# Kernel tuning notes

Hardware: AMD Instinct MI355X
Metric: run time of the kernel (lower is better)

The kernel has to match this reference:

```python
import jax, jax.numpy as jnp
import numpy as np

EMB = 128
N_RBF = 16
N_EDGES = 1_000_000
N_ATOMS = 50_000


def setup_inputs() -> dict:
    key = jax.random.key(0)
    ks = jax.random.split(key, 16)
    inp = {
        "x": jax.random.normal(ks[0], (N_EDGES, EMB), dtype=jnp.float32),
        "rbf": jax.random.normal(ks[1], (N_EDGES, N_RBF), dtype=jnp.float32),
        "idnb_i": jax.random.randint(ks[2], (N_EDGES,), 0, N_ATOMS, dtype=jnp.int32),
        "n_atoms": N_ATOMS,
        # learned params
        "W_x": jax.random.normal(ks[3], (EMB, EMB), dtype=jnp.float32) * 0.05,
        "b_x": jnp.zeros((EMB,), dtype=jnp.float32),
        "W_rbf": jax.random.normal(ks[4], (N_RBF, EMB), dtype=jnp.float32) * 0.2,
        "b_rbf": jnp.zeros((EMB,), dtype=jnp.float32),
        "W1": jax.random.normal(ks[5], (EMB, EMB), dtype=jnp.float32) * 0.05,
        "b1": jnp.zeros((EMB,), dtype=jnp.float32),
        "W2": jax.random.normal(ks[6], (EMB, EMB), dtype=jnp.float32) * 0.05,
        "b2": jnp.zeros((EMB,), dtype=jnp.float32),
        "W3": jax.random.normal(ks[7], (EMB, EMB), dtype=jnp.float32) * 0.05,
        "b3": jnp.zeros((EMB,), dtype=jnp.float32),
        "W_final": jax.random.normal(ks[8], (EMB, 1), dtype=jnp.float32) * 0.05,
        # scale coefficients (shape [1] as in the keras layer)
        "coef_rbf_a": jnp.exp(jax.random.normal(ks[9], (1,)) * 0.01),
        "coef_rbf_b": jnp.exp(jax.random.normal(ks[10], (1,)) * 0.01),
        "coef_x": jnp.exp(jax.random.normal(ks[11], (1,)) * 0.01),
        "coef_final": jnp.exp(jax.random.normal(ks[12], (1,)) * 0.01),
    }
    return inp


def reference(x, rbf, idnb_i, n_atoms, W_x, b_x, W_rbf, b_rbf, W1, b1, W2, b2,
              W3, b3, W_final, coef_rbf_a, coef_rbf_b, coef_x, coef_final):
    act = jax.nn.silu  # keras 'swish'
    rbf = coef_rbf_a * rbf
    h = act(x @ W_x + b_x)                      # [E, emb]
    g = act(rbf @ W_rbf + b_rbf)                # [E, emb]
    conv_x = (coef_rbf_b * g) * (coef_x * h)    # fused elementwise gate
    a = jax.ops.segment_sum(conv_x, idnb_i, num_segments=n_atoms)  # [n_atoms, emb]
    a = act(a @ W1 + b1)
    a = act(a @ W2 + b2)
    a = act(a @ W3 + b3)
    out = (a @ W_final) * coef_final            # [n_atoms, 1]
    return out
```

## Files before the change

### kernel.cpp

```cpp
#include <hip/hip_runtime.h>

#define E_TOTAL 1000000
#define EMB     128
#define NRBF    16
#define NATOMS  50000
#define APB     16
#define NBLK    ((NATOMS + 255) / 256)

typedef _Float16 f16x8 __attribute__((ext_vector_type(8)));
typedef _Float16 f16x4 __attribute__((ext_vector_type(4)));
typedef float    f32x4 __attribute__((ext_vector_type(4)));

__device__ __forceinline__ float silu_f(float v) {
    return v * (1.0f / (1.0f + __expf(-v)));
}

__device__ __forceinline__ int sigma64(int e) {
    return (((e & 15) >> 2) << 4) + ((e >> 4) << 2) + (e & 3);
}

__global__ __launch_bounds__(256)
void hist_kernel(const int* __restrict__ idnb, int* __restrict__ counts) {
    const int e = blockIdx.x * 256 + threadIdx.x;
    if (e < E_TOTAL) atomicAdd(&counts[idnb[e]], 1);
}

__global__ __launch_bounds__(256)
void scan1_kernel(const int* __restrict__ counts, int* __restrict__ row_ptr,
                  int* __restrict__ bsums) {
    __shared__ int sd[256];
    const int tid = threadIdx.x;
    const int idx = blockIdx.x * 256 + tid;
    const int v = (idx < NATOMS) ? counts[idx] : 0;
    sd[tid] = v;
    __syncthreads();
#pragma unroll
    for (int off = 1; off < 256; off <<= 1) {
        const int t = (tid >= off) ? sd[tid - off] : 0;
        __syncthreads();
        sd[tid] += t;
        __syncthreads();
    }
    if (idx < NATOMS) row_ptr[idx] = sd[tid] - v;
    if (tid == 255) bsums[blockIdx.x] = sd[255];
}

__global__ __launch_bounds__(256)
void scan2_kernel(int* __restrict__ bsums) {
    __shared__ int sd[256];
    const int tid = threadIdx.x;
    const int v = (tid < NBLK) ? bsums[tid] : 0;
    sd[tid] = v;
    __syncthreads();
#pragma unroll
    for (int off = 1; off < 256; off <<= 1) {
        const int t = (tid >= off) ? sd[tid - off] : 0;
        __syncthreads();
        sd[tid] += t;
        __syncthreads();
    }
    if (tid < NBLK) bsums[tid] = sd[tid] - v;
}

__global__ __launch_bounds__(256)
void scan3_kernel(const int* __restrict__ bsums, int* __restrict__ row_ptr,
                  int* __restrict__ cursor) {
    const int idx = blockIdx.x * 256 + threadIdx.x;
    if (idx < NATOMS) {
        const int r = row_ptr[idx] + bsums[blockIdx.x];
        row_ptr[idx] = r;
        cursor[idx]  = r;
    }
    if (idx == 0) row_ptr[NATOMS] = E_TOTAL;
}

__global__ __launch_bounds__(256)
void scatter_kernel(const int* __restrict__ idnb, int* __restrict__ cursor,
                    int* __restrict__ eidx) {
    const int e = blockIdx.x * 256 + threadIdx.x;
    if (e < E_TOTAL) {
        const int a = idnb[e];
        const int p = atomicAdd(&cursor[a], 1);
        eidx[p] = e;
    }
}

__global__ __launch_bounds__(256, 2)
void edge_kernel(const float* __restrict__ x,
                 const float* __restrict__ rbf,
                 const int*   __restrict__ eidx,
                 const int*   __restrict__ row_ptr,
                 const float* __restrict__ Wx,
                 const float* __restrict__ bx,
                 const float* __restrict__ Wr,
                 const float* __restrict__ br,
                 const float* __restrict__ c_a,
                 const float* __restrict__ c_b,
                 const float* __restrict__ c_x,
                 float* __restrict__ acc)
{
    __shared__ _Float16 sX[64 * 128];
    __shared__ _Float16 sR[64 * 40];
    __shared__ float    sAcc[APB][132];
    __shared__ int      sAid[64];

    const int tid  = threadIdx.x;
    const int w    = tid >> 6;
    const int lane = tid & 63;
    const int lq   = lane >> 4;
    const int lm   = lane & 15;

    const int aBase = blockIdx.x * APB;

    int rp[APB];
#pragma unroll
    for (int a = 0; a < APB; ++a) rp[a] = row_ptr[aBase + a];
    const int eBeg = rp[0];
    const int eEnd = row_ptr[aBase + APB];
    const int nEdge = eEnd - eBeg;
    const int ntile = (nEdge + 63) >> 6;

    const float ca = c_a[0];
    const float sc = c_b[0] * c_x[0];
    const int col0 = w * 32 + lm;
    const int col1 = col0 + 16;
    const float bx0 = bx[col0], bx1 = bx[col1];
    const float br0 = br[col0], br1 = br[col1];

    f16x8 wxh[4][2], wxl[4][2], wrh[2], wrl[2];
#pragma unroll
    for (int ks = 0; ks < 4; ++ks)
#pragma unroll
        for (int nt = 0; nt < 2; ++nt) {
            const int n = w * 32 + nt * 16 + lm;
            f16x8 h8, l8;
#pragma unroll
            for (int j = 0; j < 8; ++j) {
                const int k = ks * 32 + lq * 8 + j;
                const float v = Wx[k * EMB + n];
                const _Float16 hv = (_Float16)v;
                h8[j] = hv;
                l8[j] = (_Float16)(v - (float)hv);
            }
            wxh[ks][nt] = h8;
            wxl[ks][nt] = l8;
        }
#pragma unroll
    for (int nt = 0; nt < 2; ++nt) {
        const int n = w * 32 + nt * 16 + lm;
        f16x8 h8, l8;
#pragma unroll
        for (int j = 0; j < 8; ++j) {
            const int k = lq * 8 + j;
            const float v = (k < NRBF) ? Wr[k * EMB + n] : 0.f;
            const _Float16 hv = (_Float16)v;
            h8[j] = hv;
            l8[j] = (_Float16)(v - (float)hv);
        }
        wrh[nt] = h8;
        wrl[nt] = l8;
    }

    for (int f = tid; f < APB * 132; f += 256) ((float*)sAcc)[f] = 0.f;
    for (int f = tid; f < 64 * 24; f += 256)
        sR[(f / 24) * 40 + 16 + (f % 24)] = (_Float16)0.f;

    float4 px[8];
    float4 pr;
    int    prel = -1;

    auto prefetch = [&](int t) {
        const int nb = eBeg + t * 64;
#pragma unroll
        for (int i = 0; i < 8; ++i) {
            const int e = (tid >> 5) + i * 8;
            const int eid = eidx[min(nb + sigma64(e), eEnd - 1)];
            px[i] = *(const float4*)(x + (size_t)eid * EMB + (tid & 31) * 4);
        }
        {
            const int er = tid >> 2;
            const int eid = eidx[min(nb + sigma64(er), eEnd - 1)];
            pr = *(const float4*)(rbf + (size_t)eid * NRBF + (tid & 3) * 4);
        }
        if (tid < 64) {
            const int pos = nb + tid;
            if (pos >= eEnd) {
                prel = -1;
            } else {
                int rel = 0;
#pragma unroll
                for (int a = 1; a < APB; ++a) rel += (pos >= rp[a]) ? 1 : 0;
                prel = rel;
            }
        }
    };

    auto write_lds = [&]() {
#pragma unroll
        for (int i = 0; i < 8; ++i) {
            const int e = (tid >> 5) + i * 8;
            const int kb = (tid & 31) * 4;
            const int idx = (e * 128 + kb) ^ ((e & 7) << 3);
            f16x4 h4 = {(_Float16)px[i].x, (_Float16)px[i].y,
                        (_Float16)px[i].z, (_Float16)px[i].w};
            *(f16x4*)&sX[idx] = h4;
        }
        {
            const int er = tid >> 2;
            const int kb = (tid & 3) * 4;
            f16x4 r4 = {(_Float16)(pr.x * ca), (_Float16)(pr.y * ca),
                        (_Float16)(pr.z * ca), (_Float16)(pr.w * ca)};
            *(f16x4*)&sR[er * 40 + kb] = r4;
        }
        if (tid < 64) sAid[tid] = prel;
    };

    if (ntile > 0) prefetch(0);

    for (int t = 0; t < ntile; ++t) {
        __syncthreads();
        write_lds();
        __syncthreads();
        if (t + 1 < ntile) prefetch(t + 1);

        int   curA = -2;
        float a0v = 0.f, a1v = 0.f;

        auto epi = [&](const f32x4 hac[2], const f32x4 gac[2], int mt) {
            const int pbase = lq * 16 + mt * 4;
            float v0[4], v1[4];
#pragma unroll
            for (int r = 0; r < 4; ++r) {
                const float g0 = gac[0][r] + br0, h0 = hac[0][r] + bx0;
                const float g1 = gac[1][r] + br1, h1 = hac[1][r] + bx1;
                const float d0 = (1.f + __expf(-g0)) * (1.f + __expf(-h0));
                const float d1 = (1.f + __expf(-g1)) * (1.f + __expf(-h1));
                v0[r] = sc * g0 * h0 * __builtin_amdgcn_rcpf(d0);
                v1[r] = sc * g1 * h1 * __builtin_amdgcn_rcpf(d1);
            }
#pragma unroll
            for (int r = 0; r < 4; ++r) {
                const int rel = sAid[pbase + r];
                if (rel != curA) {
                    if (curA >= 0) {
                        atomicAdd(&sAcc[curA][col0], a0v);
                        atomicAdd(&sAcc[curA][col1], a1v);
                    }
                    curA = rel; a0v = 0.f; a1v = 0.f;
                }
                a0v += v0[r];
                a1v += v1[r];
            }
        };

        auto mfma_mt = [&](f32x4 hac[2], f32x4 gac[2], int mt) {
#pragma unroll
            for (int nt = 0; nt < 2; ++nt) { hac[nt] = 0.f; gac[nt] = 0.f; }
            const int m = mt * 16 + lm;
            const f16x8 rh = *(const f16x8*)&sR[m * 40 + lq * 8];
#pragma unroll
            for (int nt = 0; nt < 2; ++nt) {
                gac[nt] = __builtin_amdgcn_mfma_f32_16x16x32_f16(rh, wrh[nt], gac[nt], 0, 0, 0);
                gac[nt] = __builtin_amdgcn_mfma_f32_16x16x32_f16(rh, wrl[nt], gac[nt], 0, 0, 0);
            }
#pragma unroll
            for (int ks = 0; ks < 4; ++ks) {
                const int xi = (m * 128 + ks * 32 + lq * 8) ^ ((m & 7) << 3);
                const f16x8 xh = *(const f16x8*)&sX[xi];
#pragma unroll
                for (int nt = 0; nt < 2; ++nt) {
                    hac[nt] = __builtin_amdgcn_mfma_f32_16x16x32_f16(xh, wxh[ks][nt], hac[nt], 0, 0, 0);
                    hac[nt] = __builtin_amdgcn_mfma_f32_16x16x32_f16(xh, wxl[ks][nt], hac[nt], 0, 0, 0);
                }
            }
        };

#pragma unroll
        for (int g = 0; g < 2; ++g) {
            f32x4 hacA[2], gacA[2], hacB[2], gacB[2];
            mfma_mt(hacA, gacA, g * 2);
            mfma_mt(hacB, gacB, g * 2 + 1);
            epi(hacA, gacA, g * 2);
            epi(hacB, gacB, g * 2 + 1);
        }

        if (curA >= 0) {
            atomicAdd(&sAcc[curA][col0], a0v);
            atomicAdd(&sAcc[curA][col1], a1v);
        }
    }

    __syncthreads();
    {
        const int r = tid >> 4;
        const int c = (tid & 15) * 8;
        float* dst = acc + (size_t)(aBase + r) * EMB + c;
        *(float4*)(dst)     = *(const float4*)&sAcc[r][c];
        *(float4*)(dst + 4) = *(const float4*)&sAcc[r][c + 4];
    }
}

__global__ __launch_bounds__(256, 2)
void layer_kernel(const float* __restrict__ X,
                  const float* __restrict__ W,
                  const float* __restrict__ b,
                  float* __restrict__ Y, int M)
{
    __shared__ _Float16 sX[64 * 128];

    const int tid  = threadIdx.x;
    const int w    = tid >> 6;
    const int lane = tid & 63;
    const int lq   = lane >> 4;
    const int lm   = lane & 15;

    const int col0 = w * 32 + lm;
    const int col1 = col0 + 16;
    const float b0 = b[col0], b1 = b[col1];

    f16x8 wh[4][2], wl[4][2];
#pragma unroll
    for (int ks = 0; ks < 4; ++ks)
#pragma unroll
        for (int nt = 0; nt < 2; ++nt) {
            const int n = w * 32 + nt * 16 + lm;
            f16x8 h8, l8;
#pragma unroll
            for (int j = 0; j < 8; ++j) {
                const int k = ks * 32 + lq * 8 + j;
                const float v = W[k * EMB + n];
                const _Float16 hv = (_Float16)v;
                h8[j] = hv;
                l8[j] = (_Float16)(v - (float)hv);
            }
            wh[ks][nt] = h8;
            wl[ks][nt] = l8;
        }

#pragma unroll
    for (int sub = 0; sub < 2; ++sub) {
        const int base = blockIdx.x * 128 + sub * 64;
        __syncthreads();
#pragma unroll
        for (int i = 0; i < 8; ++i) {
            const int e = (tid >> 5) + i * 8;
            const int row = min(base + e, M - 1);
            const float4 v = *(const float4*)(X + (size_t)row * EMB + (tid & 31) * 4);
            const int kb = (tid & 31) * 4;
            const int idx = (e * 128 + kb) ^ ((e & 7) << 3);
            f16x4 h4 = {(_Float16)v.x, (_Float16)v.y, (_Float16)v.z, (_Float16)v.w};
            *(f16x4*)&sX[idx] = h4;
        }
        __syncthreads();

#pragma unroll
        for (int mth = 0; mth < 2; ++mth) {
            f32x4 hac[2][2];
#pragma unroll
            for (int mi = 0; mi < 2; ++mi)
#pragma unroll
                for (int nt = 0; nt < 2; ++nt) hac[mi][nt] = 0.f;

#pragma unroll
            for (int mi = 0; mi < 2; ++mi) {
                const int m = (mth * 2 + mi) * 16 + lm;
#pragma unroll
                for (int ks = 0; ks < 4; ++ks) {
                    const int xi = (m * 128 + ks * 32 + lq * 8) ^ ((m & 7) << 3);
                    const f16x8 xh = *(const f16x8*)&sX[xi];
#pragma unroll
                    for (int nt = 0; nt < 2; ++nt) {
                        hac[mi][nt] = __builtin_amdgcn_mfma_f32_16x16x32_f16(xh, wh[ks][nt], hac[mi][nt], 0, 0, 0);
                        hac[mi][nt] = __builtin_amdgcn_mfma_f32_16x16x32_f16(xh, wl[ks][nt], hac[mi][nt], 0, 0, 0);
                    }
                }
            }
#pragma unroll
            for (int mi = 0; mi < 2; ++mi) {
                const int rb = base + (mth * 2 + mi) * 16 + lq * 4;
#pragma unroll
                for (int r = 0; r < 4; ++r) {
                    const int row = rb + r;
                    if (row < M) {
                        Y[(size_t)row * EMB + col0] = silu_f(hac[mi][0][r] + b0);
                        Y[(size_t)row * EMB + col1] = silu_f(hac[mi][1][r] + b1);
                    }
                }
            }
        }
    }
}

__global__ __launch_bounds__(256, 2)
void layer3_final_kernel(const float* __restrict__ X,
                         const float* __restrict__ W,
                         const float* __restrict__ b,
                         const float* __restrict__ Wf,
                         const float* __restrict__ cf,
                         float* __restrict__ out, int M)
{
    __shared__ _Float16 sX[64 * 128];
    __shared__ float    sOut[128];

    const int tid  = threadIdx.x;
    const int w    = tid >> 6;
    const int lane = tid & 63;
    const int lq   = lane >> 4;
    const int lm   = lane & 15;

    const int col0 = w * 32 + lm;
    const int col1 = col0 + 16;
    const float b0 = b[col0], b1 = b[col1];
    const float wf0 = Wf[col0], wf1 = Wf[col1];
    const float cfv = cf[0];

    if (tid < 128) sOut[tid] = 0.f;

    f16x8 wh[4][2], wl[4][2];
#pragma unroll
    for (int ks = 0; ks < 4; ++ks)
#pragma unroll
        for (int nt = 0; nt < 2; ++nt) {
            const int n = w * 32 + nt * 16 + lm;
            f16x8 h8, l8;
#pragma unroll
            for (int j = 0; j < 8; ++j) {
                const int k = ks * 32 + lq * 8 + j;
                const float v = W[k * EMB + n];
                const _Float16 hv = (_Float16)v;
                h8[j] = hv;
                l8[j] = (_Float16)(v - (float)hv);
            }
            wh[ks][nt] = h8;
            wl[ks][nt] = l8;
        }

#pragma unroll
    for (int sub = 0; sub < 2; ++sub) {
        const int base = blockIdx.x * 128 + sub * 64;
        __syncthreads();
#pragma unroll
        for (int i = 0; i < 8; ++i) {
            const int e = (tid >> 5) + i * 8;
            const int row = min(base + e, M - 1);
            const float4 v = *(const float4*)(X + (size_t)row * EMB + (tid & 31) * 4);
            const int kb = (tid & 31) * 4;
            const int idx = (e * 128 + kb) ^ ((e & 7) << 3);
            f16x4 h4 = {(_Float16)v.x, (_Float16)v.y, (_Float16)v.z, (_Float16)v.w};
            *(f16x4*)&sX[idx] = h4;
        }
        __syncthreads();

#pragma unroll
        for (int mth = 0; mth < 2; ++mth) {
            f32x4 hac[2][2];
#pragma unroll
            for (int mi = 0; mi < 2; ++mi)
#pragma unroll
                for (int nt = 0; nt < 2; ++nt) hac[mi][nt] = 0.f;

#pragma unroll
            for (int mi = 0; mi < 2; ++mi) {
                const int m = (mth * 2 + mi) * 16 + lm;
#pragma unroll
                for (int ks = 0; ks < 4; ++ks) {
                    const int xi = (m * 128 + ks * 32 + lq * 8) ^ ((m & 7) << 3);
                    const f16x8 xh = *(const f16x8*)&sX[xi];
#pragma unroll
                    for (int nt = 0; nt < 2; ++nt) {
                        hac[mi][nt] = __builtin_amdgcn_mfma_f32_16x16x32_f16(xh, wh[ks][nt], hac[mi][nt], 0, 0, 0);
                        hac[mi][nt] = __builtin_amdgcn_mfma_f32_16x16x32_f16(xh, wl[ks][nt], hac[mi][nt], 0, 0, 0);
                    }
                }
            }
#pragma unroll
            for (int mi = 0; mi < 2; ++mi) {
                const int lrow = sub * 64 + (mth * 2 + mi) * 16 + lq * 4;
#pragma unroll
                for (int r = 0; r < 4; ++r) {
                    const float o0 = silu_f(hac[mi][0][r] + b0);
                    const float o1 = silu_f(hac[mi][1][r] + b1);
                    float p = o0 * wf0 + o1 * wf1;
#pragma unroll
                    for (int off = 1; off < 16; off <<= 1)
                        p += __shfl_xor(p, off);
                    if (lm == 0 && base + (mth * 2 + mi) * 16 + lq * 4 + r < M)
                        atomicAdd(&sOut[lrow + r], p);
                }
            }
        }
    }

    __syncthreads();
    if (tid < 128) {
        const int row = blockIdx.x * 128 + tid;
        if (row < M) out[row] = sOut[tid] * cfv;
    }
}

extern "C" void kernel_launch(void* const* d_in, const int* in_sizes, int n_in,
                              void* d_out, int out_size, void* d_ws, size_t ws_size,
                              hipStream_t stream) {
    const float* x    = (const float*)d_in[0];
    const float* rbf  = (const float*)d_in[1];
    const int*   idnb = (const int*)  d_in[2];
    const float* Wx   = (const float*)d_in[4];
    const float* bx   = (const float*)d_in[5];
    const float* Wr   = (const float*)d_in[6];
    const float* brf  = (const float*)d_in[7];
    const float* W1   = (const float*)d_in[8];
    const float* b1   = (const float*)d_in[9];
    const float* W2   = (const float*)d_in[10];
    const float* b2   = (const float*)d_in[11];
    const float* W3   = (const float*)d_in[12];
    const float* b3   = (const float*)d_in[13];
    const float* Wf   = (const float*)d_in[14];
    const float* c_a  = (const float*)d_in[15];
    const float* c_b  = (const float*)d_in[16];
    const float* c_x  = (const float*)d_in[17];
    const float* c_f  = (const float*)d_in[18];

    float* out = (float*)d_out;
    float* acc = (float*)d_ws;
    float* buf = acc + (size_t)NATOMS * EMB;
    int* eidx    = (int*)buf;
    int* counts  = eidx + E_TOTAL;
    int* row_ptr = counts + NATOMS;
    int* cursor  = row_ptr + NATOMS + 1;
    int* bsums   = cursor + NATOMS;

    hipMemsetAsync(counts, 0, NATOMS * sizeof(int), stream);

    hist_kernel<<<(E_TOTAL + 255) / 256, 256, 0, stream>>>(idnb, counts);
    scan1_kernel<<<NBLK, 256, 0, stream>>>(counts, row_ptr, bsums);
    scan2_kernel<<<1, 256, 0, stream>>>(bsums);
    scan3_kernel<<<NBLK, 256, 0, stream>>>(bsums, row_ptr, cursor);
    scatter_kernel<<<(E_TOTAL + 255) / 256, 256, 0, stream>>>(idnb, cursor, eidx);

    edge_kernel<<<NATOMS / APB, 256, 0, stream>>>(x, rbf, eidx, row_ptr,
                                                  Wx, bx, Wr, brf,
                                                  c_a, c_b, c_x, acc);

    const int ltiles = (NATOMS + 127) / 128;
    layer_kernel<<<ltiles, 256, 0, stream>>>(acc, W1, b1, buf, NATOMS);
    layer_kernel<<<ltiles, 256, 0, stream>>>(buf, W2, b2, acc, NATOMS);
    layer3_final_kernel<<<ltiles, 256, 0, stream>>>(acc, W3, b3, Wf, c_f, out, NATOMS);
}
```

Measured before the change: 399.4 us.

## Deepen edge-kernel prefetch pipeline, cache edge indices in LDS, drop rbf low split

```diff
diff --git a/kernel.cpp b/kernel.cpp
--- a/kernel.cpp
+++ b/kernel.cpp
@@ -6,6 +6,7 @@
 #define NATOMS  50000
 #define APB     16
 #define NBLK    ((NATOMS + 255) / 256)
+#define EIDX_CACHE 1280
 
 typedef _Float16 f16x8 __attribute__((ext_vector_type(8)));
 typedef _Float16 f16x4 __attribute__((ext_vector_type(4)));
@@ -85,7 +86,7 @@
     }
 }
 
-__global__ __launch_bounds__(256, 2)
+__global__ __launch_bounds__(256)
 void edge_kernel(const float* __restrict__ x,
                  const float* __restrict__ rbf,
                  const int*   __restrict__ eidx,
@@ -102,6 +103,7 @@
     __shared__ _Float16 sX[64 * 128];
     __shared__ _Float16 sR[64 * 40];
     __shared__ float    sAcc[APB][132];
+    __shared__ int      sEidx[EIDX_CACHE];
     __shared__ int      sAid[64];
 
     const int tid  = threadIdx.x;
@@ -109,6 +111,8 @@
     const int lane = tid & 63;
     const int lq   = lane >> 4;
     const int lm   = lane & 15;
+    const int row  = tid >> 2;
+    const int gcb  = tid & 3;
 
     const int aBase = blockIdx.x * APB;
 
@@ -127,7 +131,7 @@
     const float bx0 = bx[col0], bx1 = bx[col1];
     const float br0 = br[col0], br1 = br[col1];
 
-    f16x8 wxh[4][2], wxl[4][2], wrh[2], wrl[2];
+    f16x8 wxh[4][2], wxl[4][2], wrh[2];
 #pragma unroll
     for (int ks = 0; ks < 4; ++ks)
 #pragma unroll
@@ -148,39 +152,59 @@
 #pragma unroll
     for (int nt = 0; nt < 2; ++nt) {
         const int n = w * 32 + nt * 16 + lm;
-        f16x8 h8, l8;
+        f16x8 h8;
 #pragma unroll
         for (int j = 0; j < 8; ++j) {
             const int k = lq * 8 + j;
-            const float v = (k < NRBF) ? Wr[k * EMB + n] : 0.f;
-            const _Float16 hv = (_Float16)v;
-            h8[j] = hv;
-            l8[j] = (_Float16)(v - (float)hv);
+            h8[j] = (_Float16)((k < NRBF) ? Wr[k * EMB + n] : 0.f);
         }
         wrh[nt] = h8;
-        wrl[nt] = l8;
     }
 
     for (int f = tid; f < APB * 132; f += 256) ((float*)sAcc)[f] = 0.f;
     for (int f = tid; f < 64 * 24; f += 256)
         sR[(f / 24) * 40 + 16 + (f % 24)] = (_Float16)0.f;
+    for (int f = tid; f < EIDX_CACHE; f += 256)
+        sEidx[f] = (f < nEdge) ? eidx[eBeg + f] : 0;
+    __syncthreads();
 
     float4 px[8];
-    float4 pr;
+    f16x8  pxh[4];
+    f16x4  prh;
     int    prel = -1;
 
-    auto prefetch = [&](int t) {
+    auto issue = [&](int t) {
         const int nb = eBeg + t * 64;
-#pragma unroll
-        for (int i = 0; i < 8; ++i) {
-            const int e = (tid >> 5) + i * 8;
-            const int eid = eidx[min(nb + sigma64(e), eEnd - 1)];
-            px[i] = *(const float4*)(x + (size_t)eid * EMB + (tid & 31) * 4);
-        }
+        int p = nb + sigma64(row);
+        p = min(p, eEnd - 1);
+        const int off = p - eBeg;
+        const int eid = (off < EIDX_CACHE) ? sEidx[off] : eidx[p];
+        const float* xr = x + (size_t)eid * EMB;
+#pragma unroll
+        for (int i = 0; i < 4; ++i) {
+            const int k0 = (gcb + 4 * i) * 8;
+            px[2 * i]     = *(const float4*)(xr + k0);
+            px[2 * i + 1] = *(const float4*)(xr + k0 + 4);
+        }
+    };
+
+    auto convert = [&](int t) {
+        const int nb = eBeg + t * 64;
         {
-            const int er = tid >> 2;
-            const int eid = eidx[min(nb + sigma64(er), eEnd - 1)];
-            pr = *(const float4*)(rbf + (size_t)eid * NRBF + (tid & 3) * 4);
+            int p = nb + sigma64(row);
+            p = min(p, eEnd - 1);
+            const int off = p - eBeg;
+            const int eid = (off < EIDX_CACHE) ? sEidx[off] : eidx[p];
+            const float4 pr = *(const float4*)(rbf + (size_t)eid * NRBF + gcb * 4);
+            prh = f16x4{(_Float16)(pr.x * ca), (_Float16)(pr.y * ca),
+                        (_Float16)(pr.z * ca), (_Float16)(pr.w * ca)};
+        }
+#pragma unroll
+        for (int i = 0; i < 4; ++i) {
+            const float4 a = px[2 * i];
+            const float4 b = px[2 * i + 1];
+            pxh[i] = f16x8{(_Float16)a.x, (_Float16)a.y, (_Float16)a.z, (_Float16)a.w,
+                           (_Float16)b.x, (_Float16)b.y, (_Float16)b.z, (_Float16)b.w};
         }
         if (tid < 64) {
             const int pos = nb + tid;
@@ -197,31 +221,29 @@
 
     auto write_lds = [&]() {
 #pragma unroll
-        for (int i = 0; i < 8; ++i) {
-            const int e = (tid >> 5) + i * 8;
-            const int kb = (tid & 31) * 4;
-            const int idx = (e * 128 + kb) ^ ((e & 7) << 3);
-            f16x4 h4 = {(_Float16)px[i].x, (_Float16)px[i].y,
-                        (_Float16)px[i].z, (_Float16)px[i].w};
-            *(f16x4*)&sX[idx] = h4;
-        }
-        {
-            const int er = tid >> 2;
-            const int kb = (tid & 3) * 4;
-            f16x4 r4 = {(_Float16)(pr.x * ca), (_Float16)(pr.y * ca),
-                        (_Float16)(pr.z * ca), (_Float16)(pr.w * ca)};
-            *(f16x4*)&sR[er * 40 + kb] = r4;
-        }
+        for (int i = 0; i < 4; ++i) {
+            const int gc = gcb + 4 * i;
+            const int idx = (row * 128 + gc * 8) ^ ((row & 7) << 3);
+            *(f16x8*)&sX[idx] = pxh[i];
+        }
+        *(f16x4*)&sR[row * 40 + gcb * 4] = prh;
         if (tid < 64) sAid[tid] = prel;
     };
 
-    if (ntile > 0) prefetch(0);
+    if (ntile > 0) {
+        issue(0);
+        convert(0);
+        if (ntile > 1) issue(1);
+    }
 
     for (int t = 0; t < ntile; ++t) {
-        __syncthreads();
         write_lds();
         __syncthreads();
-        if (t + 1 < ntile) prefetch(t + 1);
+
+        if (t + 1 < ntile) {
+            convert(t + 1);
+            if (t + 2 < ntile) issue(t + 2);
+        }
 
         int   curA = -2;
         float a0v = 0.f, a1v = 0.f;
@@ -259,10 +281,8 @@
             const int m = mt * 16 + lm;
             const f16x8 rh = *(const f16x8*)&sR[m * 40 + lq * 8];
 #pragma unroll
-            for (int nt = 0; nt < 2; ++nt) {
+            for (int nt = 0; nt < 2; ++nt)
                 gac[nt] = __builtin_amdgcn_mfma_f32_16x16x32_f16(rh, wrh[nt], gac[nt], 0, 0, 0);
-                gac[nt] = __builtin_amdgcn_mfma_f32_16x16x32_f16(rh, wrl[nt], gac[nt], 0, 0, 0);
-            }
 #pragma unroll
             for (int ks = 0; ks < 4; ++ks) {
                 const int xi = (m * 128 + ks * 32 + lq * 8) ^ ((m & 7) << 3);
@@ -288,9 +308,10 @@
             atomicAdd(&sAcc[curA][col0], a0v);
             atomicAdd(&sAcc[curA][col1], a1v);
         }
-    }
-
-    __syncthreads();
+
+        __syncthreads();
+    }
+
     {
         const int r = tid >> 4;
         const int c = (tid & 15) * 8;
@@ -344,8 +365,8 @@
 #pragma unroll
         for (int i = 0; i < 8; ++i) {
             const int e = (tid >> 5) + i * 8;
-            const int row = min(base + e, M - 1);
-            const float4 v = *(const float4*)(X + (size_t)row * EMB + (tid & 31) * 4);
+            const int rowg = min(base + e, M - 1);
+            const float4 v = *(const float4*)(X + (size_t)rowg * EMB + (tid & 31) * 4);
             const int kb = (tid & 31) * 4;
             const int idx = (e * 128 + kb) ^ ((e & 7) << 3);
             f16x4 h4 = {(_Float16)v.x, (_Float16)v.y, (_Float16)v.z, (_Float16)v.w};
@@ -380,10 +401,10 @@
                 const int rb = base + (mth * 2 + mi) * 16 + lq * 4;
 #pragma unroll
                 for (int r = 0; r < 4; ++r) {
-                    const int row = rb + r;
-                    if (row < M) {
-                        Y[(size_t)row * EMB + col0] = silu_f(hac[mi][0][r] + b0);
-                        Y[(size_t)row * EMB + col1] = silu_f(hac[mi][1][r] + b1);
+                    const int rowg = rb + r;
+                    if (rowg < M) {
+                        Y[(size_t)rowg * EMB + col0] = silu_f(hac[mi][0][r] + b0);
+                        Y[(size_t)rowg * EMB + col1] = silu_f(hac[mi][1][r] + b1);
                     }
                 }
             }
@@ -442,8 +463,8 @@
 #pragma unroll
         for (int i = 0; i < 8; ++i) {
             const int e = (tid >> 5) + i * 8;
-            const int row = min(base + e, M - 1);
-            const float4 v = *(const float4*)(X + (size_t)row * EMB + (tid & 31) * 4);
+            const int rowg = min(base + e, M - 1);
+            const float4 v = *(const float4*)(X + (size_t)rowg * EMB + (tid & 31) * 4);
             const int kb = (tid & 31) * 4;
             const int idx = (e * 128 + kb) ^ ((e & 7) << 3);
             f16x4 h4 = {(_Float16)v.x, (_Float16)v.y, (_Float16)v.z, (_Float16)v.w};
@@ -493,8 +514,8 @@
 
     __syncthreads();
     if (tid < 128) {
-        const int row = blockIdx.x * 128 + tid;
-        if (row < M) out[row] = sOut[tid] * cfv;
+        const int rowg = blockIdx.x * 128 + tid;
+        if (rowg < M) out[rowg] = sOut[tid] * cfv;
     }
 }
 
```

Result: slower. 430.1 us (+7.7%).

## Fuse three MLP layers into one kernel and raise atoms per edge block

Applied to the files above, without the earlier changes.

```diff
diff --git a/kernel.cpp b/kernel.cpp
--- a/kernel.cpp
+++ b/kernel.cpp
@@ -4,7 +4,7 @@
 #define EMB     128
 #define NRBF    16
 #define NATOMS  50000
-#define APB     16
+#define APB     40
 #define NBLK    ((NATOMS + 255) / 256)
 
 typedef _Float16 f16x8 __attribute__((ext_vector_type(8)));
@@ -291,22 +291,29 @@
     }
 
     __syncthreads();
-    {
-        const int r = tid >> 4;
-        const int c = (tid & 15) * 8;
-        float* dst = acc + (size_t)(aBase + r) * EMB + c;
-        *(float4*)(dst)     = *(const float4*)&sAcc[r][c];
-        *(float4*)(dst + 4) = *(const float4*)&sAcc[r][c + 4];
+#pragma unroll
+    for (int it = 0; it < 3; ++it) {
+        const int r = (tid >> 4) + it * 16;
+        if (r < APB) {
+            const int c = (tid & 15) * 8;
+            float* dst = acc + (size_t)(aBase + r) * EMB + c;
+            *(float4*)(dst)     = *(const float4*)&sAcc[r][c];
+            *(float4*)(dst + 4) = *(const float4*)&sAcc[r][c + 4];
+        }
     }
 }
 
 __global__ __launch_bounds__(256, 2)
-void layer_kernel(const float* __restrict__ X,
-                  const float* __restrict__ W,
-                  const float* __restrict__ b,
-                  float* __restrict__ Y, int M)
+void mlp_fused_kernel(const float* __restrict__ X,
+                      const float* __restrict__ W1, const float* __restrict__ b1,
+                      const float* __restrict__ W2, const float* __restrict__ b2,
+                      const float* __restrict__ W3, const float* __restrict__ b3,
+                      const float* __restrict__ Wf, const float* __restrict__ cf,
+                      float* __restrict__ out, int M)
 {
-    __shared__ _Float16 sX[64 * 128];
+    __shared__ _Float16 sA[128 * 128];
+    __shared__ _Float16 sB[128 * 128];
+    __shared__ float    sOut[128];
 
     const int tid  = threadIdx.x;
     const int w    = tid >> 6;
@@ -314,186 +321,114 @@
     const int lq   = lane >> 4;
     const int lm   = lane & 15;
 
+    const int base = blockIdx.x * 128;
     const int col0 = w * 32 + lm;
     const int col1 = col0 + 16;
-    const float b0 = b[col0], b1 = b[col1];
-
-    f16x8 wh[4][2], wl[4][2];
-#pragma unroll
-    for (int ks = 0; ks < 4; ++ks)
-#pragma unroll
-        for (int nt = 0; nt < 2; ++nt) {
-            const int n = w * 32 + nt * 16 + lm;
-            f16x8 h8, l8;
-#pragma unroll
-            for (int j = 0; j < 8; ++j) {
-                const int k = ks * 32 + lq * 8 + j;
-                const float v = W[k * EMB + n];
-                const _Float16 hv = (_Float16)v;
-                h8[j] = hv;
-                l8[j] = (_Float16)(v - (float)hv);
-            }
-            wh[ks][nt] = h8;
-            wl[ks][nt] = l8;
-        }
-
-#pragma unroll
-    for (int sub = 0; sub < 2; ++sub) {
-        const int base = blockIdx.x * 128 + sub * 64;
-        __syncthreads();
-#pragma unroll
-        for (int i = 0; i < 8; ++i) {
-            const int e = (tid >> 5) + i * 8;
-            const int row = min(base + e, M - 1);
-            const float4 v = *(const float4*)(X + (size_t)row * EMB + (tid & 31) * 4);
-            const int kb = (tid & 31) * 4;
-            const int idx = (e * 128 + kb) ^ ((e & 7) << 3);
-            f16x4 h4 = {(_Float16)v.x, (_Float16)v.y, (_Float16)v.z, (_Float16)v.w};
-            *(f16x4*)&sX[idx] = h4;
-        }
-        __syncthreads();
-
-#pragma unroll
-        for (int mth = 0; mth < 2; ++mth) {
-            f32x4 hac[2][2];
-#pragma unroll
-            for (int mi = 0; mi < 2; ++mi)
-#pragma unroll
-                for (int nt = 0; nt < 2; ++nt) hac[mi][nt] = 0.f;
-
-#pragma unroll
-            for (int mi = 0; mi < 2; ++mi) {
-                const int m = (mth * 2 + mi) * 16 + lm;
-#pragma unroll
-                for (int ks = 0; ks < 4; ++ks) {
-                    const int xi = (m * 128 + ks * 32 + lq * 8) ^ ((m & 7) << 3);
-                    const f16x8 xh = *(const f16x8*)&sX[xi];
-#pragma unroll
-                    for (int nt = 0; nt < 2; ++nt) {
-                        hac[mi][nt] = __builtin_amdgcn_mfma_f32_16x16x32_f16(xh, wh[ks][nt], hac[mi][nt], 0, 0, 0);
-                        hac[mi][nt] = __builtin_amdgcn_mfma_f32_16x16x32_f16(xh, wl[ks][nt], hac[mi][nt], 0, 0, 0);
+    const float wf0 = Wf[col0], wf1 = Wf[col1];
+    const float cfv = cf[0];
+
+    if (tid < 128) sOut[tid] = 0.f;
+
+#pragma unroll
+    for (int i = 0; i < 16; ++i) {
+        const int e = (tid >> 5) + i * 8;
+        const int row = min(base + e, M - 1);
+        const float4 v = *(const float4*)(X + (size_t)row * EMB + (tid & 31) * 4);
+        const int kb = (tid & 31) * 4;
+        const int idx = (e * 128 + kb) ^ ((e & 7) << 3);
+        f16x4 h4 = {(_Float16)v.x, (_Float16)v.y, (_Float16)v.z, (_Float16)v.w};
+        *(f16x4*)&sA[idx] = h4;
+    }
+    __syncthreads();
+
+    const float* Ws[3] = {W1, W2, W3};
+    const float* bs[3] = {b1, b2, b3};
+
+#pragma unroll 1
+    for (int L = 0; L < 3; ++L) {
+        const _Float16* sIn   = (L & 1) ? sB : sA;
+        _Float16*       sDst  = (L & 1) ? sA : sB;
+        const float*    W     = Ws[L];
+        const float     bb0   = bs[L][col0];
+        const float     bb1   = bs[L][col1];
+
+        f16x8 wh[4][2], wl[4][2];
+#pragma unroll
+        for (int ks = 0; ks < 4; ++ks)
+#pragma unroll
+            for (int nt = 0; nt < 2; ++nt) {
+                const int n = w * 32 + nt * 16 + lm;
+                f16x8 h8, l8;
+#pragma unroll
+                for (int j = 0; j < 8; ++j) {
+                    const int k = ks * 32 + lq * 8 + j;
+                    const float v = W[k * EMB + n];
+                    const _Float16 hv = (_Float16)v;
+                    h8[j] = hv;
+                    l8[j] = (_Float16)(v - (float)hv);
+                }
+                wh[ks][nt] = h8;
+                wl[ks][nt] = l8;
+            }
+
+#pragma unroll
+        for (int sub = 0; sub < 2; ++sub) {
+#pragma unroll
+            for (int mth = 0; mth < 2; ++mth) {
+                f32x4 hac[2][2];
+#pragma unroll
+                for (int mi = 0; mi < 2; ++mi)
+#pragma unroll
+                    for (int nt = 0; nt < 2; ++nt) hac[mi][nt] = 0.f;
+
+#pragma unroll
+                for (int mi = 0; mi < 2; ++mi) {
+                    const int m = sub * 64 + (mth * 2 + mi) * 16 + lm;
+#pragma unroll
+                    for (int ks = 0; ks < 4; ++ks) {
+                        const int xi = (m * 128 + ks * 32 + lq * 8) ^ ((m & 7) << 3);
+                        const f16x8 xh = *(const f16x8*)&sIn[xi];
+#pragma unroll
+                        for (int nt = 0; nt < 2; ++nt) {
+                            hac[mi][nt] = __builtin_amdgcn_mfma_f32_16x16x32_f16(xh, wh[ks][nt], hac[mi][nt], 0, 0, 0);
+                            hac[mi][nt] = __builtin_amdgcn_mfma_f32_16x16x32_f16(xh, wl[ks][nt], hac[mi][nt], 0, 0, 0);
+                        }
                     }
                 }
-            }
-#pragma unroll
-            for (int mi = 0; mi < 2; ++mi) {
-                const int rb = base + (mth * 2 + mi) * 16 + lq * 4;
-#pragma unroll
-                for (int r = 0; r < 4; ++r) {
-                    const int row = rb + r;
-                    if (row < M) {
-                        Y[(size_t)row * EMB + col0] = silu_f(hac[mi][0][r] + b0);
-                        Y[(size_t)row * EMB + col1] = silu_f(hac[mi][1][r] + b1);
+
+#pragma unroll
+                for (int mi = 0; mi < 2; ++mi) {
+                    const int rowl = sub * 64 + (mth * 2 + mi) * 16 + lq * 4;
+                    if (L < 2) {
+#pragma unroll
+                        for (int r = 0; r < 4; ++r) {
+                            const float o0 = silu_f(hac[mi][0][r] + bb0);
+                            const float o1 = silu_f(hac[mi][1][r] + bb1);
+                            const int rw = rowl + r;
+                            sDst[(rw * 128 + col0) ^ ((rw & 7) << 3)] = (_Float16)o0;
+                            sDst[(rw * 128 + col1) ^ ((rw & 7) << 3)] = (_Float16)o1;
+                        }
+                    } else {
+#pragma unroll
+                        for (int r = 0; r < 4; ++r) {
+                            const float o0 = silu_f(hac[mi][0][r] + bb0);
+                            const float o1 = silu_f(hac[mi][1][r] + bb1);
+                            float p = o0 * wf0 + o1 * wf1;
+#pragma unroll
+                            for (int off = 1; off < 16; off <<= 1)
+                                p += __shfl_xor(p, off);
+                            if (lm == 0 && base + rowl + r < M)
+                                atomicAdd(&sOut[rowl + r], p);
+                        }
                     }
                 }
             }
         }
-    }
-}
-
-__global__ __launch_bounds__(256, 2)
-void layer3_final_kernel(const float* __restrict__ X,
-                         const float* __restrict__ W,
-                         const float* __restrict__ b,
-                         const float* __restrict__ Wf,
-                         const float* __restrict__ cf,
-                         float* __restrict__ out, int M)
-{
-    __shared__ _Float16 sX[64 * 128];
-    __shared__ float    sOut[128];
-
-    const int tid  = threadIdx.x;
-    const int w    = tid >> 6;
-    const int lane = tid & 63;
-    const int lq   = lane >> 4;
-    const int lm   = lane & 15;
-
-    const int col0 = w * 32 + lm;
-    const int col1 = col0 + 16;
-    const float b0 = b[col0], b1 = b[col1];
-    const float wf0 = Wf[col0], wf1 = Wf[col1];
-    const float cfv = cf[0];
-
-    if (tid < 128) sOut[tid] = 0.f;
-
-    f16x8 wh[4][2], wl[4][2];
-#pragma unroll
-    for (int ks = 0; ks < 4; ++ks)
-#pragma unroll
-        for (int nt = 0; nt < 2; ++nt) {
-            const int n = w * 32 + nt * 16 + lm;
-            f16x8 h8, l8;
-#pragma unroll
-            for (int j = 0; j < 8; ++j) {
-                const int k = ks * 32 + lq * 8 + j;
-                const float v = W[k * EMB + n];
-                const _Float16 hv = (_Float16)v;
-                h8[j] = hv;
-                l8[j] = (_Float16)(v - (float)hv);
-            }
-            wh[ks][nt] = h8;
-            wl[ks][nt] = l8;
-        }
-
-#pragma unroll
-    for (int sub = 0; sub < 2; ++sub) {
-        const int base = blockIdx.x * 128 + sub * 64;
-        __syncthreads();
-#pragma unroll
-        for (int i = 0; i < 8; ++i) {
-            const int e = (tid >> 5) + i * 8;
-            const int row = min(base + e, M - 1);
-            const float4 v = *(const float4*)(X + (size_t)row * EMB + (tid & 31) * 4);
-            const int kb = (tid & 31) * 4;
-            const int idx = (e * 128 + kb) ^ ((e & 7) << 3);
-            f16x4 h4 = {(_Float16)v.x, (_Float16)v.y, (_Float16)v.z, (_Float16)v.w};
-            *(f16x4*)&sX[idx] = h4;
-        }
-        __syncthreads();
-
-#pragma unroll
-        for (int mth = 0; mth < 2; ++mth) {
-            f32x4 hac[2][2];
-#pragma unroll
-            for (int mi = 0; mi < 2; ++mi)
-#pragma unroll
-                for (int nt = 0; nt < 2; ++nt) hac[mi][nt] = 0.f;
-
-#pragma unroll
-            for (int mi = 0; mi < 2; ++mi) {
-                const int m = (mth * 2 + mi) * 16 + lm;
-#pragma unroll
-                for (int ks = 0; ks < 4; ++ks) {
-                    const int xi = (m * 128 + ks * 32 + lq * 8) ^ ((m & 7) << 3);
-                    const f16x8 xh = *(const f16x8*)&sX[xi];
-#pragma unroll
-                    for (int nt = 0; nt < 2; ++nt) {
-                        hac[mi][nt] = __builtin_amdgcn_mfma_f32_16x16x32_f16(xh, wh[ks][nt], hac[mi][nt], 0, 0, 0);
-                        hac[mi][nt] = __builtin_amdgcn_mfma_f32_16x16x32_f16(xh, wl[ks][nt], hac[mi][nt], 0, 0, 0);
-                    }
-                }
-            }
-#pragma unroll
-            for (int mi = 0; mi < 2; ++mi) {
-                const int lrow = sub * 64 + (mth * 2 + mi) * 16 + lq * 4;
-#pragma unroll
-                for (int r = 0; r < 4; ++r) {
-                    const float o0 = silu_f(hac[mi][0][r] + b0);
-                    const float o1 = silu_f(hac[mi][1][r] + b1);
-                    float p = o0 * wf0 + o1 * wf1;
-#pragma unroll
-                    for (int off = 1; off < 16; off <<= 1)
-                        p += __shfl_xor(p, off);
-                    if (lm == 0 && base + (mth * 2 + mi) * 16 + lq * 4 + r < M)
-                        atomicAdd(&sOut[lrow + r], p);
-                }
-            }
-        }
-    }
-
-    __syncthreads();
+        __syncthreads();
+    }
+
     if (tid < 128) {
-        const int row = blockIdx.x * 128 + tid;
+        const int row = base + tid;
         if (row < M) out[row] = sOut[tid] * cfv;
     }
 }
@@ -541,8 +476,6 @@
                                                   Wx, bx, Wr, brf,
                                                   c_a, c_b, c_x, acc);
 
-    const int ltiles = (NATOMS + 127) / 128;
-    layer_kernel<<<ltiles, 256, 0, stream>>>(acc, W1, b1, buf, NATOMS);
-    layer_kernel<<<ltiles, 256, 0, stream>>>(buf, W2, b2, acc, NATOMS);
-    layer3_final_kernel<<<ltiles, 256, 0, stream>>>(acc, W3, b3, Wf, c_f, out, NATOMS);
-}
+    mlp_fused_kernel<<<(NATOMS + 127) / 128, 256, 0, stream>>>(
+        acc, W1, b1, W2, b2, W3, b3, Wf, c_f, out, NATOMS);
+}
```

Measured after the change: 380.1 us. 1.05x faster.
